# Kernel optimization log

Measured on AMD Instinct MI355X. Metric: run time of the kernel, lower is better.

The kernel has to match this reference:

```python
import jax, jax.numpy as jnp
import numpy as np

B, N, E0, F_IN, H, EMB, VEC, DPI = 1024, 256, 2048, 6, 32, 32, 26, 512


def setup_inputs() -> dict:
    key = jax.random.key(0)
    ks = jax.random.split(key, 16)
    # fixed urban scene graph, shared by every batch element, with self-loops
    src0 = jax.random.randint(ks[0], (E0,), 0, N, dtype=jnp.int32)
    dst0 = jax.random.randint(ks[1], (E0,), 0, N, dtype=jnp.int32)
    loops = jnp.arange(N, dtype=jnp.int32)
    src = jnp.concatenate([src0, loops])
    dst = jnp.concatenate([dst0, loops])

    s = 0.05
    return {
        "graph_feats": jax.random.normal(ks[2], (B, N, F_IN), jnp.float32),
        "vector": jax.random.normal(ks[3], (B, VEC), jnp.float32),
        "src": src,
        "dst": dst,
        "W1": jax.random.normal(ks[4], (F_IN, H), jnp.float32) * s,
        "b1": jnp.zeros((H,), jnp.float32),
        "W2": jax.random.normal(ks[5], (H, H), jnp.float32) * s,
        "b2": jnp.zeros((H,), jnp.float32),
        "W3": jax.random.normal(ks[6], (H, H), jnp.float32) * s,
        "b3": jnp.zeros((H,), jnp.float32),
        "W_emb": jax.random.normal(ks[7], (H, EMB), jnp.float32) * s,
        "b_emb": jnp.zeros((EMB,), jnp.float32),
        "W_pi": jax.random.normal(ks[8], (VEC + EMB, DPI), jnp.float32) * s,
        "b_pi": jnp.zeros((DPI,), jnp.float32),
        "W_vf": jax.random.normal(ks[9], (VEC + EMB, DPI), jnp.float32) * s,
        "b_vf": jnp.zeros((DPI,), jnp.float32),
    }


def _edge_norm(src, dst, n_nodes):
    # DGL GraphConv norm='both': out_deg(src)^-1/2 * in_deg(dst)^-1/2
    ones = jnp.ones(src.shape[0], jnp.float32)
    deg_out = jax.ops.segment_sum(ones, src, num_segments=n_nodes)
    deg_in = jax.ops.segment_sum(ones, dst, num_segments=n_nodes)
    inv_o = jnp.where(deg_out > 0, deg_out ** -0.5, 0.0)
    inv_i = jnp.where(deg_in > 0, deg_in ** -0.5, 0.0)
    return inv_o[src] * inv_i[dst]  # [E]


def _gconv(h, src, dst, norm, W, b):
    # h: [B, N, F]; symmetric-normalized aggregation then linear (DGL GraphConv)
    msg = h[:, src, :] * norm[None, :, None]          # [B, E, F]
    agg = jnp.zeros_like(h).at[:, dst, :].add(msg)     # [B, N, F]
    return agg @ W + b


def reference(graph_feats, vector, src, dst, W1, b1, W2, b2, W3, b3,
              W_emb, b_emb, W_pi, b_pi, W_vf, b_vf):
    n_nodes = graph_feats.shape[1]
    norm = _edge_norm(src, dst, n_nodes)
    h = jax.nn.relu(_gconv(graph_feats, src, dst, norm, W1, b1))
    h = jax.nn.relu(_gconv(h, src, dst, norm, W2, b2))
    h = jax.nn.relu(_gconv(h, src, dst, norm, W3, b3))  # three_layers=True
    hg = jnp.mean(h, axis=1)                 # dgl.mean_nodes -> [B, H]
    emb = hg @ W_emb + b_emb                 # [B, EMB]
    comb = jnp.concatenate([vector[:, :26], emb], axis=1)  # [B, 58]
    pi = jax.nn.relu(comb @ W_pi + b_pi)
    vf = jax.nn.relu(comb @ W_vf + b_vf)
    return pi, vf
```

## Files before the change

### kernel.cpp

```cpp
#include <hip/hip_runtime.h>
#include <hip/hip_fp16.h>

#define B_    1024
#define N_    256
#define E_    2304
#define EPT_  9
#define FIN_  6
#define VEC_  26
#define HSTR_ 40

typedef _Float16 half8 __attribute__((ext_vector_type(8)));
typedef float    f32x4 __attribute__((ext_vector_type(4)));

__global__ __launch_bounds__(256) void fused_kernel(
    const float* __restrict__ gf,
    const float* __restrict__ vec,
    const int* __restrict__ src, const int* __restrict__ dst,
    const float* __restrict__ W1, const float* __restrict__ b1,
    const float* __restrict__ W2, const float* __restrict__ b2,
    const float* __restrict__ W3, const float* __restrict__ b3,
    const float* __restrict__ We, const float* __restrict__ be,
    const float* __restrict__ Wpi, const float* __restrict__ bpi,
    const float* __restrict__ Wvf, const float* __restrict__ bvf,
    float2* __restrict__ out)
{
    __shared__ __align__(16) __half hbuf[N_ * HSTR_];
    __shared__ unsigned int packedE[E_];
    __shared__ float part[8 * 33];
    __shared__ float hgl[32];
    __shared__ float comb[VEC_ + 32];
    __shared__ int   wsum[4];

    const int t = threadIdx.x;
    const int b = blockIdx.x;
    const int lane = t & 63, wv = t >> 6;

    int*   deg_o  = (int*)hbuf;
    int*   deg_i  = (int*)hbuf + 256;
    int*   scanA  = (int*)hbuf + 512;
    int*   cursor = (int*)hbuf + 768;
    int*   perm   = (int*)hbuf + 1024;
    float* inv_o  = (float*)hbuf + 1280;
    float* inv_i  = (float*)hbuf + 1536;
    int*   bcnt   = (int*)hbuf + 1792;
    int*   boff   = (int*)hbuf + 1856;

    deg_o[t] = 0; deg_i[t] = 0;
    if (t < 64) bcnt[t] = 0;
    __syncthreads();

    int sB[EPT_], dB[EPT_];
#pragma unroll
    for (int i = 0; i < EPT_; ++i) { int e = t + 256 * i; sB[i] = src[e]; dB[i] = dst[e]; }
#pragma unroll
    for (int i = 0; i < EPT_; ++i) { atomicAdd(&deg_o[sB[i]], 1); atomicAdd(&deg_i[dB[i]], 1); }
    __syncthreads();

    const int dI = deg_i[t];
    {
        int dO = deg_o[t];
        inv_o[t] = dO > 0 ? rsqrtf((float)dO) : 0.f;
        inv_i[t] = dI > 0 ? rsqrtf((float)dI) : 0.f;
    }
    int x = dI;
#pragma unroll
    for (int d = 1; d < 64; d <<= 1) {
        int y = __shfl_up(x, d, 64);
        if (lane >= d) x += y;
    }
    if (lane == 63) wsum[wv] = x;
    const int bucket = dI > 63 ? 63 : dI;
    atomicAdd(&bcnt[bucket], 1);
    __syncthreads();

    {
        int prefix = 0;
#pragma unroll
        for (int w = 0; w < 3; ++w) if (w < wv) prefix += wsum[w];
        int incl = x + prefix;
        scanA[t]  = incl;
        cursor[t] = incl - dI;
    }
    if (t < 64) {
        int c = bcnt[t], xx = c;
#pragma unroll
        for (int d = 1; d < 64; d <<= 1) {
            int y = __shfl_up(xx, d, 64);
            if (lane >= d) xx += y;
        }
        boff[t] = xx - c;
    }
    __syncthreads();

    { int pos = atomicAdd(&boff[bucket], 1); perm[pos] = t; }
#pragma unroll
    for (int i = 0; i < EPT_; ++i) {
        int s = sB[i], dd = dB[i];
        int pos = atomicAdd(&cursor[dd], 1);
        float nrm = inv_o[s] * inv_i[dd];
        unsigned short h = __half_as_ushort(__float2half(nrm));
        packedE[pos] = ((unsigned int)s << 16) | (unsigned int)h;
    }
    __syncthreads();

    const int node = perm[t];
    const int end  = scanA[node];
    const int beg  = end - deg_i[node];
    __syncthreads();

    {
        const float* g = gf + (size_t)b * (N_ * FIN_);
        for (int i = t; i < N_ * 8; i += 256) {
            int n = i >> 3, k = i & 7;
            hbuf[n * HSTR_ + k] = __float2half((k < FIN_) ? g[n * FIN_ + k] : 0.f);
        }
    }
    __syncthreads();

    const __half2 z2 = __float2half2_rn(0.f);

    {
        __half2 a2[4] = {z2, z2, z2, z2};
        for (int e = beg; e < end; ++e) {
            unsigned int u = packedE[e];
            __half2 w2 = __half2half2(__ushort_as_half((unsigned short)(u & 0xffffu)));
            union { float4 f4; __half2 h2[4]; } r;
            r.f4 = *(const float4*)&hbuf[(u >> 16) * HSTR_];
#pragma unroll
            for (int q = 0; q < 4; ++q) a2[q] = __hfma2(w2, r.h2[q], a2[q]);
        }
        float a[FIN_], o[32];
#pragma unroll
        for (int k = 0; k < FIN_; ++k)
            a[k] = (k & 1) ? __high2float(a2[k >> 1]) : __low2float(a2[k >> 1]);
#pragma unroll
        for (int j = 0; j < 32; ++j) o[j] = b1[j];
#pragma unroll
        for (int k = 0; k < FIN_; ++k) {
            float ak = a[k];
            const float* wr = &W1[k * 32];
#pragma unroll
            for (int j = 0; j < 32; ++j) o[j] += ak * wr[j];
        }
        __syncthreads();
        union { float4 f4; __half2 h2[4]; } w;
        float4* row = (float4*)&hbuf[node * HSTR_];
#pragma unroll
        for (int q = 0; q < 4; ++q) {
#pragma unroll
            for (int r = 0; r < 4; ++r)
                w.h2[r] = __floats2half2_rn(fmaxf(o[8*q + 2*r], 0.f), fmaxf(o[8*q + 2*r + 1], 0.f));
            row[q] = w.f4;
        }
    }
    __syncthreads();

    const int m16  = lane & 15;
    const int q4   = lane >> 4;
    const int slab = wv * 64;

    for (int L = 0; L < 2; ++L) {
        const float* Wl = (L == 0) ? W2 : W3;
        const float* Bl = (L == 0) ? b2 : b3;

        half8 bfrag[2];
        float bias_c[2];
#pragma unroll
        for (int h = 0; h < 2; ++h) {
            int col = m16 + 16 * h;
#pragma unroll
            for (int j = 0; j < 8; ++j)
                bfrag[h][j] = (_Float16)Wl[(q4 * 8 + j) * 32 + col];
            bias_c[h] = Bl[col];
        }

        __half2 acc2[16];
#pragma unroll
        for (int j = 0; j < 16; ++j) acc2[j] = z2;
        for (int e = beg; e < end; ++e) {
            unsigned int u = packedE[e];
            __half2 w2 = __half2half2(__ushort_as_half((unsigned short)(u & 0xffffu)));
            const float4* hr = (const float4*)&hbuf[(u >> 16) * HSTR_];
            union { float4 f4; __half2 h2[4]; } r0, r1, r2, r3;
            r0.f4 = hr[0]; r1.f4 = hr[1]; r2.f4 = hr[2]; r3.f4 = hr[3];
#pragma unroll
            for (int q = 0; q < 4; ++q) {
                acc2[q]      = __hfma2(w2, r0.h2[q], acc2[q]);
                acc2[4 + q]  = __hfma2(w2, r1.h2[q], acc2[4 + q]);
                acc2[8 + q]  = __hfma2(w2, r2.h2[q], acc2[8 + q]);
                acc2[12 + q] = __hfma2(w2, r3.h2[q], acc2[12 + q]);
            }
        }
        __syncthreads();
        {
            union { float4 f4; __half2 h2[4]; } w;
            float4* row = (float4*)&hbuf[node * HSTR_];
#pragma unroll
            for (int q = 0; q < 4; ++q) {
#pragma unroll
                for (int r = 0; r < 4; ++r) w.h2[r] = acc2[4 * q + r];
                row[q] = w.f4;
            }
        }
        __syncthreads();

        half8 afrag[4];
#pragma unroll
        for (int g = 0; g < 4; ++g) {
            union { float4 f4; half8 h8; } u;
            u.f4 = *(const float4*)&hbuf[(slab + g * 16 + m16) * HSTR_ + q4 * 8];
            afrag[g] = u.h8;
        }
        f32x4 D[4][2];
#pragma unroll
        for (int g = 0; g < 4; ++g) {
#pragma unroll
            for (int h = 0; h < 2; ++h) {
                f32x4 c = {bias_c[h], bias_c[h], bias_c[h], bias_c[h]};
                D[g][h] = __builtin_amdgcn_mfma_f32_16x16x32_f16(afrag[g], bfrag[h], c, 0, 0, 0);
            }
        }
#pragma unroll
        for (int g = 0; g < 4; ++g) {
#pragma unroll
            for (int h = 0; h < 2; ++h) {
#pragma unroll
                for (int r = 0; r < 4; ++r) {
                    float v = fmaxf(D[g][h][r], 0.f);
                    hbuf[(slab + g * 16 + q4 * 4 + r) * HSTR_ + h * 16 + m16] = __float2half(v);
                }
            }
        }
        __syncthreads();
    }

    {
        int j = t & 31, g8 = t >> 5;
        float s = 0.f;
        for (int i = 0; i < 32; ++i)
            s += __half2float(hbuf[(g8 * 32 + i) * HSTR_ + j]);
        part[g8 * 33 + j] = s;
    }
    __syncthreads();
    if (t < 32) {
        float sum = 0.f;
#pragma unroll
        for (int g8 = 0; g8 < 8; ++g8) sum += part[g8 * 33 + t];
        hgl[t] = sum * (1.0f / 256.0f);
    }
    __syncthreads();

    if (t < 32) {
        float v = be[t];
#pragma unroll
        for (int j = 0; j < 32; ++j) v += hgl[j] * We[j * 32 + t];
        comb[VEC_ + t] = v;
    }
    if (t < VEC_) comb[t] = vec[b * VEC_ + t];
    __syncthreads();

    {
        float p0 = bpi[2 * t], p1 = bpi[2 * t + 1];
        float v0 = bvf[2 * t], v1 = bvf[2 * t + 1];
        const float2* Wp = (const float2*)Wpi;
        const float2* Wv = (const float2*)Wvf;
        for (int k = 0; k < VEC_ + 32; ++k) {
            float c = comb[k];
            float2 a = Wp[k * 256 + t];
            p0 += c * a.x; p1 += c * a.y;
            float2 d = Wv[k * 256 + t];
            v0 += c * d.x; v1 += c * d.y;
        }
        out[b * 256 + t]          = make_float2(fmaxf(p0, 0.f), fmaxf(p1, 0.f));
        out[262144 + b * 256 + t] = make_float2(fmaxf(v0, 0.f), fmaxf(v1, 0.f));
    }
}

extern "C" void kernel_launch(void* const* d_in, const int* in_sizes, int n_in,
                              void* d_out, int out_size, void* d_ws, size_t ws_size,
                              hipStream_t stream)
{
    fused_kernel<<<B_, 256, 0, stream>>>(
        (const float*)d_in[0], (const float*)d_in[1],
        (const int*)d_in[2], (const int*)d_in[3],
        (const float*)d_in[4], (const float*)d_in[5],
        (const float*)d_in[6], (const float*)d_in[7],
        (const float*)d_in[8], (const float*)d_in[9],
        (const float*)d_in[10], (const float*)d_in[11],
        (const float*)d_in[12], (const float*)d_in[13],
        (const float*)d_in[14], (const float*)d_in[15],
        (float2*)d_out);
}
```

Measured before the change: 117.2 us.

## Double block size to 512 threads, splitting each node's edge gather across thread pairs

Launches 512 threads per block and assigns two threads to each node. Each thread accumulates alternate incoming edges, and a shuffle-based pair sum combines the two halves. The MFMA stage now gives each wave 32 rows instead of 64, and the pooling and output-projection stages are re-split so each thread handles one output element. The aim is more parallelism per block to hide LDS gather latency, at the cost of extra shuffles, idle threads during the setup phases, and possibly lower occupancy from the larger block.

```diff
diff --git a/kernel.cpp b/kernel.cpp
--- a/kernel.cpp
+++ b/kernel.cpp
@@ -4,15 +4,22 @@
 #define B_    1024
 #define N_    256
 #define E_    2304
-#define EPT_  9
 #define FIN_  6
 #define VEC_  26
 #define HSTR_ 40
+#define NT_   512
 
 typedef _Float16 half8 __attribute__((ext_vector_type(8)));
 typedef float    f32x4 __attribute__((ext_vector_type(4)));
 
-__global__ __launch_bounds__(256) void fused_kernel(
+__device__ __forceinline__ __half2 pairsum(__half2 v) {
+    union { __half2 h; int i; } u; u.h = v;
+    int p = __shfl_xor(u.i, 1, 64);
+    union { int i; __half2 h; } w; w.i = p;
+    return __hfma2(w.h, __floats2half2_rn(1.f, 1.f), v);
+}
+
+__global__ __launch_bounds__(512) void fused_kernel(
     const float* __restrict__ gf,
     const float* __restrict__ vec,
     const int* __restrict__ src, const int* __restrict__ dst,
@@ -22,11 +29,11 @@
     const float* __restrict__ We, const float* __restrict__ be,
     const float* __restrict__ Wpi, const float* __restrict__ bpi,
     const float* __restrict__ Wvf, const float* __restrict__ bvf,
-    float2* __restrict__ out)
+    float* __restrict__ out)
 {
     __shared__ __align__(16) __half hbuf[N_ * HSTR_];
     __shared__ unsigned int packedE[E_];
-    __shared__ float part[8 * 33];
+    __shared__ float part[16 * 33];
     __shared__ float hgl[32];
     __shared__ float comb[VEC_ + 32];
     __shared__ int   wsum[4];
@@ -34,6 +41,7 @@
     const int t = threadIdx.x;
     const int b = blockIdx.x;
     const int lane = t & 63, wv = t >> 6;
+    const int sub = t & 1;
 
     int*   deg_o  = (int*)hbuf;
     int*   deg_i  = (int*)hbuf + 256;
@@ -45,35 +53,35 @@
     int*   bcnt   = (int*)hbuf + 1792;
     int*   boff   = (int*)hbuf + 1856;
 
-    deg_o[t] = 0; deg_i[t] = 0;
+    if (t < 256) { deg_o[t] = 0; deg_i[t] = 0; }
     if (t < 64) bcnt[t] = 0;
     __syncthreads();
 
-    int sB[EPT_], dB[EPT_];
-#pragma unroll
-    for (int i = 0; i < EPT_; ++i) { int e = t + 256 * i; sB[i] = src[e]; dB[i] = dst[e]; }
-#pragma unroll
-    for (int i = 0; i < EPT_; ++i) { atomicAdd(&deg_o[sB[i]], 1); atomicAdd(&deg_i[dB[i]], 1); }
-    __syncthreads();
-
-    const int dI = deg_i[t];
-    {
+    for (int e = t; e < E_; e += NT_) {
+        atomicAdd(&deg_o[src[e]], 1);
+        atomicAdd(&deg_i[dst[e]], 1);
+    }
+    __syncthreads();
+
+    int x = 0, dI = 0, bucket = 0;
+    if (t < 256) {
+        dI = deg_i[t];
         int dO = deg_o[t];
         inv_o[t] = dO > 0 ? rsqrtf((float)dO) : 0.f;
         inv_i[t] = dI > 0 ? rsqrtf((float)dI) : 0.f;
-    }
-    int x = dI;
-#pragma unroll
-    for (int d = 1; d < 64; d <<= 1) {
-        int y = __shfl_up(x, d, 64);
-        if (lane >= d) x += y;
-    }
-    if (lane == 63) wsum[wv] = x;
-    const int bucket = dI > 63 ? 63 : dI;
-    atomicAdd(&bcnt[bucket], 1);
-    __syncthreads();
-
-    {
+        x = dI;
+#pragma unroll
+        for (int d = 1; d < 64; d <<= 1) {
+            int y = __shfl_up(x, d, 64);
+            if (lane >= d) x += y;
+        }
+        if (lane == 63) wsum[wv] = x;
+        bucket = dI > 63 ? 63 : dI;
+        atomicAdd(&bcnt[bucket], 1);
+    }
+    __syncthreads();
+
+    if (t < 256) {
         int prefix = 0;
 #pragma unroll
         for (int w = 0; w < 3; ++w) if (w < wv) prefix += wsum[w];
@@ -92,10 +100,9 @@
     }
     __syncthreads();
 
-    { int pos = atomicAdd(&boff[bucket], 1); perm[pos] = t; }
-#pragma unroll
-    for (int i = 0; i < EPT_; ++i) {
-        int s = sB[i], dd = dB[i];
+    if (t < 256) { int pos = atomicAdd(&boff[bucket], 1); perm[pos] = t; }
+    for (int e = t; e < E_; e += NT_) {
+        int s = src[e], dd = dst[e];
         int pos = atomicAdd(&cursor[dd], 1);
         float nrm = inv_o[s] * inv_i[dd];
         unsigned short h = __half_as_ushort(__float2half(nrm));
@@ -103,14 +110,14 @@
     }
     __syncthreads();
 
-    const int node = perm[t];
+    const int node = perm[t >> 1];
     const int end  = scanA[node];
     const int beg  = end - deg_i[node];
     __syncthreads();
 
     {
         const float* g = gf + (size_t)b * (N_ * FIN_);
-        for (int i = t; i < N_ * 8; i += 256) {
+        for (int i = t; i < N_ * 8; i += NT_) {
             int n = i >> 3, k = i & 7;
             hbuf[n * HSTR_ + k] = __float2half((k < FIN_) ? g[n * FIN_ + k] : 0.f);
         }
@@ -121,7 +128,7 @@
 
     {
         __half2 a2[4] = {z2, z2, z2, z2};
-        for (int e = beg; e < end; ++e) {
+        for (int e = beg + sub; e < end; e += 2) {
             unsigned int u = packedE[e];
             __half2 w2 = __half2half2(__ushort_as_half((unsigned short)(u & 0xffffu)));
             union { float4 f4; __half2 h2[4]; } r;
@@ -129,35 +136,43 @@
 #pragma unroll
             for (int q = 0; q < 4; ++q) a2[q] = __hfma2(w2, r.h2[q], a2[q]);
         }
-        float a[FIN_], o[32];
-#pragma unroll
-        for (int k = 0; k < FIN_; ++k)
-            a[k] = (k & 1) ? __high2float(a2[k >> 1]) : __low2float(a2[k >> 1]);
-#pragma unroll
-        for (int j = 0; j < 32; ++j) o[j] = b1[j];
-#pragma unroll
-        for (int k = 0; k < FIN_; ++k) {
-            float ak = a[k];
-            const float* wr = &W1[k * 32];
-#pragma unroll
-            for (int j = 0; j < 32; ++j) o[j] += ak * wr[j];
+#pragma unroll
+        for (int q = 0; q < 4; ++q) a2[q] = pairsum(a2[q]);
+
+        float o[32];
+        if (sub == 0) {
+            float a[FIN_];
+#pragma unroll
+            for (int k = 0; k < FIN_; ++k)
+                a[k] = (k & 1) ? __high2float(a2[k >> 1]) : __low2float(a2[k >> 1]);
+#pragma unroll
+            for (int j = 0; j < 32; ++j) o[j] = b1[j];
+#pragma unroll
+            for (int k = 0; k < FIN_; ++k) {
+                float ak = a[k];
+                const float* wr = &W1[k * 32];
+#pragma unroll
+                for (int j = 0; j < 32; ++j) o[j] += ak * wr[j];
+            }
         }
         __syncthreads();
-        union { float4 f4; __half2 h2[4]; } w;
-        float4* row = (float4*)&hbuf[node * HSTR_];
-#pragma unroll
-        for (int q = 0; q < 4; ++q) {
-#pragma unroll
-            for (int r = 0; r < 4; ++r)
-                w.h2[r] = __floats2half2_rn(fmaxf(o[8*q + 2*r], 0.f), fmaxf(o[8*q + 2*r + 1], 0.f));
-            row[q] = w.f4;
+        if (sub == 0) {
+            union { float4 f4; __half2 h2[4]; } w;
+            float4* row = (float4*)&hbuf[node * HSTR_];
+#pragma unroll
+            for (int q = 0; q < 4; ++q) {
+#pragma unroll
+                for (int r = 0; r < 4; ++r)
+                    w.h2[r] = __floats2half2_rn(fmaxf(o[8*q + 2*r], 0.f), fmaxf(o[8*q + 2*r + 1], 0.f));
+                row[q] = w.f4;
+            }
         }
     }
     __syncthreads();
 
     const int m16  = lane & 15;
     const int q4   = lane >> 4;
-    const int slab = wv * 64;
+    const int slab = wv * 32;
 
     for (int L = 0; L < 2; ++L) {
         const float* Wl = (L == 0) ? W2 : W3;
@@ -177,7 +192,7 @@
         __half2 acc2[16];
 #pragma unroll
         for (int j = 0; j < 16; ++j) acc2[j] = z2;
-        for (int e = beg; e < end; ++e) {
+        for (int e = beg + sub; e < end; e += 2) {
             unsigned int u = packedE[e];
             __half2 w2 = __half2half2(__ushort_as_half((unsigned short)(u & 0xffffu)));
             const float4* hr = (const float4*)&hbuf[(u >> 16) * HSTR_];
@@ -191,8 +206,10 @@
                 acc2[12 + q] = __hfma2(w2, r3.h2[q], acc2[12 + q]);
             }
         }
+#pragma unroll
+        for (int j = 0; j < 16; ++j) acc2[j] = pairsum(acc2[j]);
         __syncthreads();
-        {
+        if (sub == 0) {
             union { float4 f4; __half2 h2[4]; } w;
             float4* row = (float4*)&hbuf[node * HSTR_];
 #pragma unroll
@@ -204,16 +221,16 @@
         }
         __syncthreads();
 
-        half8 afrag[4];
-#pragma unroll
-        for (int g = 0; g < 4; ++g) {
+        half8 afrag[2];
+#pragma unroll
+        for (int g = 0; g < 2; ++g) {
             union { float4 f4; half8 h8; } u;
             u.f4 = *(const float4*)&hbuf[(slab + g * 16 + m16) * HSTR_ + q4 * 8];
             afrag[g] = u.h8;
         }
-        f32x4 D[4][2];
-#pragma unroll
-        for (int g = 0; g < 4; ++g) {
+        f32x4 D[2][2];
+#pragma unroll
+        for (int g = 0; g < 2; ++g) {
 #pragma unroll
             for (int h = 0; h < 2; ++h) {
                 f32x4 c = {bias_c[h], bias_c[h], bias_c[h], bias_c[h]};
@@ -221,7 +238,7 @@
             }
         }
 #pragma unroll
-        for (int g = 0; g < 4; ++g) {
+        for (int g = 0; g < 2; ++g) {
 #pragma unroll
             for (int h = 0; h < 2; ++h) {
 #pragma unroll
@@ -235,17 +252,17 @@
     }
 
     {
-        int j = t & 31, g8 = t >> 5;
+        int j = t & 31, g16 = t >> 5;
         float s = 0.f;
-        for (int i = 0; i < 32; ++i)
-            s += __half2float(hbuf[(g8 * 32 + i) * HSTR_ + j]);
-        part[g8 * 33 + j] = s;
+        for (int i = 0; i < 16; ++i)
+            s += __half2float(hbuf[(g16 * 16 + i) * HSTR_ + j]);
+        part[g16 * 33 + j] = s;
     }
     __syncthreads();
     if (t < 32) {
         float sum = 0.f;
 #pragma unroll
-        for (int g8 = 0; g8 < 8; ++g8) sum += part[g8 * 33 + t];
+        for (int g16 = 0; g16 < 16; ++g16) sum += part[g16 * 33 + t];
         hgl[t] = sum * (1.0f / 256.0f);
     }
     __syncthreads();
@@ -260,19 +277,14 @@
     __syncthreads();
 
     {
-        float p0 = bpi[2 * t], p1 = bpi[2 * t + 1];
-        float v0 = bvf[2 * t], v1 = bvf[2 * t + 1];
-        const float2* Wp = (const float2*)Wpi;
-        const float2* Wv = (const float2*)Wvf;
+        float p = bpi[t], v = bvf[t];
         for (int k = 0; k < VEC_ + 32; ++k) {
             float c = comb[k];
-            float2 a = Wp[k * 256 + t];
-            p0 += c * a.x; p1 += c * a.y;
-            float2 d = Wv[k * 256 + t];
-            v0 += c * d.x; v1 += c * d.y;
-        }
-        out[b * 256 + t]          = make_float2(fmaxf(p0, 0.f), fmaxf(p1, 0.f));
-        out[262144 + b * 256 + t] = make_float2(fmaxf(v0, 0.f), fmaxf(v1, 0.f));
+            p += c * Wpi[k * 512 + t];
+            v += c * Wvf[k * 512 + t];
+        }
+        out[(size_t)b * 512 + t]          = fmaxf(p, 0.f);
+        out[524288 + (size_t)b * 512 + t] = fmaxf(v, 0.f);
     }
 }
 
@@ -280,7 +292,7 @@
                               void* d_out, int out_size, void* d_ws, size_t ws_size,
                               hipStream_t stream)
 {
-    fused_kernel<<<B_, 256, 0, stream>>>(
+    fused_kernel<<<B_, NT_, 0, stream>>>(
         (const float*)d_in[0], (const float*)d_in[1],
         (const int*)d_in[2], (const int*)d_in[3],
         (const float*)d_in[4], (const float*)d_in[5],
@@ -289,5 +301,5 @@
         (const float*)d_in[10], (const float*)d_in[11],
         (const float*)d_in[12], (const float*)d_in[13],
         (const float*)d_in[14], (const float*)d_in[15],
-        (float2*)d_out);
+        (float*)d_out);
 }
```

Measured after the change: 121.9 us. 1.04x slower.
